# Kernel tuning notes

Measured on AMD Instinct MI355X. Metric: run time of the kernel, lower is better.

Reference implementation:

```python
import jax, jax.numpy as jnp
import numpy as np

B, T, C = 8, 2048, 1024
H, D = 16, 64  # n_heads, head_size; H*D == C


def setup_inputs() -> dict:
    key = jax.random.key(0)
    ks = jax.random.split(key, 6)
    s = 0.02
    x = jax.random.normal(ks[0], (B, T, C), dtype=jnp.float32)
    wq = jax.random.normal(ks[1], (H, C, D), dtype=jnp.float32) * s
    wk = jax.random.normal(ks[2], (H, C, D), dtype=jnp.float32) * s
    wv = jax.random.normal(ks[3], (H, C, D), dtype=jnp.float32) * s
    w_proj = jax.random.normal(ks[4], (H * D, C), dtype=jnp.float32) * s
    b_proj = jax.random.normal(ks[5], (C,), dtype=jnp.float32) * s
    return {"x": x, "wq": wq, "wk": wk, "wv": wv, "w_proj": w_proj, "b_proj": b_proj}


def reference(x, wq, wk, wv, w_proj, b_proj):
    Bq, Tq, Cq = x.shape
    # Batched per-head projections (original loops over heads with separate Linears)
    q = jnp.einsum('btc,hcd->bhtd', x, wq)
    k = jnp.einsum('btc,hcd->bhtd', x, wk)
    v = jnp.einsum('btc,hcd->bhtd', x, wv)
    # NOTE: source scales by C**-0.5 where C is the INPUT embed dim, not head_size
    wei = jnp.einsum('bhtd,bhsd->bhts', q, k) * (Cq ** -0.5)
    causal = jnp.tril(jnp.ones((Tq, Tq), dtype=bool))
    wei = jnp.where(causal, wei, jnp.float32(-jnp.inf))
    wei = jax.nn.softmax(wei, axis=-1)
    # dropout is identity in eval/reference mode
    out = jnp.einsum('bhts,bhsd->bhtd', wei, v)
    out = out.transpose(0, 2, 1, 3).reshape(Bq, Tq, H * D)  # concat over heads
    return out @ w_proj + b_proj
```

## Files before the change

kernel.cpp:

```cpp
#include <hip/hip_runtime.h>
#include <stdint.h>

#define DEV static __device__ __forceinline__

typedef __attribute__((ext_vector_type(8))) short bf16x8;
typedef __attribute__((ext_vector_type(4))) float f32x4;

constexpr int Bc = 8, Tc = 2048, Cc = 1024, Hc = 16, Dc = 64;

DEV ushort f2bf(float f) {
  union { float f; uint32_t u; } x{f};
  uint32_t r = (x.u + 0x7FFFu + ((x.u >> 16) & 1u)) >> 16;
  return (ushort)r;
}

DEV uint32_t cvt_pk_bf16(float a, float b) {
  uint32_t r;
  asm("v_cvt_pk_bf16_f32 %0, %1, %2" : "=v"(r) : "v"(a), "v"(b));
  return r;
}

DEV float max3f(float a, float b, float c) {
  float r;
  asm("v_max3_f32 %0, %1, %2, %3" : "=v"(r) : "v"(a), "v"(b), "v"(c));
  return r;
}

DEV void gload16(const ushort* g, ushort* l) {
  __builtin_amdgcn_global_load_lds(
      (const __attribute__((address_space(1))) unsigned int*)g,
      (__attribute__((address_space(3))) unsigned int*)l, 16, 0, 0);
}

DEV f32x4 mfma16(bf16x8 a, bf16x8 b, f32x4 c) {
  return __builtin_amdgcn_mfma_f32_16x16x32_bf16(a, b, c, 0, 0, 0);
}

union B8 { bf16x8 v; uint4 u; };

__global__ __launch_bounds__(256) void k_conv_x(const float* __restrict__ x, ushort* __restrict__ xb) {
  int i = blockIdx.x * 256 + threadIdx.x;
  float4 v = ((const float4*)x)[i];
  ushort4 o = make_ushort4(f2bf(v.x), f2bf(v.y), f2bf(v.z), f2bf(v.w));
  ((ushort4*)xb)[i] = o;
}

__global__ __launch_bounds__(256) void k_conv_wqkv(const float* __restrict__ wq, const float* __restrict__ wk,
                                                   const float* __restrict__ wv, ushort* __restrict__ wt) {
  int i = blockIdx.x * 256 + threadIdx.x;
  int c = i & 1023;
  int n = i >> 10;
  int which = n >> 10;
  int rem = n & 1023;
  int h = rem >> 6, d = rem & 63;
  const float* src = which == 0 ? wq : (which == 1 ? wk : wv);
  float v = src[((size_t)h * 1024 + c) * 64 + d];
  if (which == 0) v *= 0.03125f * 1.44269504088896340736f;
  wt[i] = f2bf(v);
}

__global__ __launch_bounds__(256) void k_conv_wproj(const float* __restrict__ wp, ushort* __restrict__ wt) {
  int i = blockIdx.x * 256 + threadIdx.x;
  int n = i >> 10, k = i & 1023;
  wt[i] = f2bf(wp[(size_t)k * 1024 + n]);
}

DEV void gemm_main(const ushort* __restrict__ A, const ushort* __restrict__ BT,
                   int m0, int n0, int tid, ushort* lds_a, ushort* lds_b,
                   f32x4 (&acc)[4][4]) {
  const int lane = tid & 63, wid = tid >> 6;
  const int lr = lane & 15, lg = lane >> 4;
  const int wm = wid >> 1, wn = wid & 1;
  for (int kt = 0; kt < 16; ++kt) {
#pragma unroll
    for (int r = 0; r < 4; ++r) {
      int flat = r * 256 + tid;
      int row = flat >> 3, c8 = flat & 7;
      gload16(&A[(size_t)(m0 + row) * 1024 + kt * 64 + c8 * 8], &lds_a[flat * 8]);
      gload16(&BT[(size_t)(n0 + row) * 1024 + kt * 64 + c8 * 8], &lds_b[flat * 8]);
    }
    __syncthreads();
#pragma unroll
    for (int kc = 0; kc < 2; ++kc) {
      bf16x8 af[4], bfr[4];
#pragma unroll
      for (int mf = 0; mf < 4; ++mf)
        af[mf] = *(const bf16x8*)&lds_a[(wm * 64 + mf * 16 + lr) * 64 + kc * 32 + lg * 8];
#pragma unroll
      for (int nf = 0; nf < 4; ++nf)
        bfr[nf] = *(const bf16x8*)&lds_b[(wn * 64 + nf * 16 + lr) * 64 + kc * 32 + lg * 8];
      __builtin_amdgcn_s_setprio(1);
#pragma unroll
      for (int mf = 0; mf < 4; ++mf)
#pragma unroll
        for (int nf = 0; nf < 4; ++nf)
          acc[mf][nf] = mfma16(af[mf], bfr[nf], acc[mf][nf]);
      __builtin_amdgcn_s_setprio(0);
    }
    __syncthreads();
  }
}

__global__ __launch_bounds__(256) void k_gemm_qkv(const ushort* __restrict__ xb, const ushort* __restrict__ wt,
                                                  ushort* __restrict__ qws, ushort* __restrict__ kws,
                                                  ushort* __restrict__ vws) {
  __shared__ ushort lds_a[128 * 64];
  __shared__ ushort lds_b[128 * 64];
  const int tid = threadIdx.x;
  const int m0 = blockIdx.y * 128, n0 = blockIdx.x * 128;
  f32x4 acc[4][4];
  f32x4 z = {0.f, 0.f, 0.f, 0.f};
  for (int i = 0; i < 4; ++i) for (int j = 0; j < 4; ++j) acc[i][j] = z;
  gemm_main(xb, wt, m0, n0, tid, lds_a, lds_b, acc);
  const int lane = tid & 63, wid = tid >> 6;
  const int lr = lane & 15, lg = lane >> 4;
  const int wm = wid >> 1, wn = wid & 1;
#pragma unroll
  for (int mf = 0; mf < 4; ++mf)
#pragma unroll
    for (int nf = 0; nf < 4; ++nf)
#pragma unroll
      for (int r = 0; r < 4; ++r) {
        int m = m0 + wm * 64 + mf * 16 + lg * 4 + r;
        int n = n0 + wn * 64 + nf * 16 + lr;
        int which = n >> 10, rem = n & 1023;
        int h = rem >> 6, d = rem & 63;
        int b = m >> 11, t = m & 2047;
        ushort* dst = which == 0 ? qws : (which == 1 ? kws : vws);
        dst[((size_t)(b * Hc + h) * Tc + t) * 64 + d] = f2bf(acc[mf][nf][r]);
      }
}

__global__ __launch_bounds__(256) void k_vtrans(const ushort* __restrict__ v, ushort* __restrict__ vt) {
  __shared__ ushort lds[64][68];
  const int t0 = blockIdx.x * 64;
  const int bh = blockIdx.y;
  const int tid = threadIdx.x;
  const ushort* src = v + (size_t)bh * Tc * 64;
  ushort* dst = vt + (size_t)bh * 64 * Tc;
#pragma unroll
  for (int j = 0; j < 4; ++j) {
    int flat = j * 256 + tid;
    int row = flat >> 4, cg = flat & 15;
    ushort4 x = *(const ushort4*)&src[(size_t)(t0 + row) * 64 + cg * 4];
    lds[row][cg * 4 + 0] = x.x; lds[row][cg * 4 + 1] = x.y;
    lds[row][cg * 4 + 2] = x.z; lds[row][cg * 4 + 3] = x.w;
  }
  __syncthreads();
#pragma unroll
  for (int j = 0; j < 4; ++j) {
    int flat = j * 256 + tid;
    int d = flat >> 4, tg = flat & 15;
    ushort4 x = make_ushort4(lds[tg * 4 + 0][d], lds[tg * 4 + 1][d], lds[tg * 4 + 2][d], lds[tg * 4 + 3][d]);
    *(ushort4*)&dst[(size_t)d * Tc + t0 + tg * 4] = x;
  }
}

DEV int swzK(int row, int bcol) { return row * 128 + (bcol ^ ((row & 7) << 4)); }
DEV int swzV(int row, int bcol) { return row * 256 + (bcol ^ ((row & 7) << 4)); }

__global__ __launch_bounds__(256) void k_attn(const ushort* __restrict__ qws, const ushort* __restrict__ kws,
                                              const ushort* __restrict__ vtws, ushort* __restrict__ att) {
  const int id = blockIdx.x;
  const int xcd = id & 7, slot = id >> 3;
  const int bh = (xcd << 4) + (slot >> 3);
  const int qi = slot & 7;
  const int tid = threadIdx.x, lane = tid & 63, wid = tid >> 6;
  const int lr = lane & 15, lg = lane >> 4;

  __shared__ __align__(16) ushort lds_k[2 * 128 * 64];
  __shared__ __align__(16) ushort lds_v[2 * 64 * 128];

  const ushort* qbase = qws + (size_t)bh * Tc * 64;
  const ushort* kbase = kws + (size_t)bh * Tc * 64;
  const ushort* vtbase = vtws + (size_t)bh * 64 * Tc;
  const int b = bh >> 4, h = bh & 15;
  const f32x4 z = {0.f, 0.f, 0.f, 0.f};

  int rowK[4], colK[4], rowV[4], colV[4];
#pragma unroll
  for (int r = 0; r < 4; ++r) {
    int c = r * 256 + tid;
    rowK[r] = c >> 3; colK[r] = 8 * ((c & 7) ^ (rowK[r] & 7));
    rowV[r] = c >> 4; colV[r] = 8 * ((c & 15) ^ (rowV[r] & 7));
  }

  B8 onesf;
  {
    uint32_t pp = lr == 0 ? 0x3F803F80u : 0u;
    onesf.u = make_uint4(pp, pp, pp, pp);
  }

  for (int pass = 0; pass < 2; ++pass) {
    const int qb = pass == 0 ? qi : 15 - qi;
    const int q0 = qb * 128;
    const int ntiles = qb + 1;
    const int qrow = q0 + wid * 32;
    const int qgmax = qrow + 31;

    bf16x8 qa[2][2];
#pragma unroll
    for (int qf = 0; qf < 2; ++qf)
#pragma unroll
      for (int kc = 0; kc < 2; ++kc)
        qa[qf][kc] = *(const bf16x8*)&qbase[(size_t)(qrow + qf * 16 + lr) * 64 + kc * 32 + lg * 8];

    f32x4 o[2][4];
    f32x4 lac[2];
    float m_[2];
#pragma unroll
    for (int qf = 0; qf < 2; ++qf) {
#pragma unroll
      for (int df = 0; df < 4; ++df) o[qf][df] = z;
      lac[qf] = z;
      m_[qf] = -1e30f;
    }

    __syncthreads();

#pragma unroll
    for (int r = 0; r < 4; ++r) {
      gload16(&kbase[(size_t)rowK[r] * 64 + colK[r]], &lds_k[(r * 256 + tid) * 8]);
      gload16(&vtbase[(size_t)rowV[r] * Tc + colV[r]], &lds_v[(r * 256 + tid) * 8]);
    }

    for (int it = 0; it < ntiles; ++it) {
      __syncthreads();
      const ushort* ldsK = lds_k + (it & 1) * 8192;
      const ushort* ldsV = lds_v + (it & 1) * 8192;
      if (it + 1 < ntiles) {
        const int s0n = (it + 1) * 128;
        ushort* dK = lds_k + ((it + 1) & 1) * 8192;
        ushort* dV = lds_v + ((it + 1) & 1) * 8192;
#pragma unroll
        for (int r = 0; r < 4; ++r) {
          gload16(&kbase[(size_t)(s0n + rowK[r]) * 64 + colK[r]], &dK[(r * 256 + tid) * 8]);
          gload16(&vtbase[(size_t)rowV[r] * Tc + s0n + colV[r]], &dV[(r * 256 + tid) * 8]);
        }
      }

      const int s0 = it * 128;
      const bool diag = (it == ntiles - 1);
      const int nlive = diag ? 2 * wid + 2 : 8;

      f32x4 s[8][2];
#pragma unroll
      for (int sf = 0; sf < 8; ++sf)
#pragma unroll
        for (int qf = 0; qf < 2; ++qf) s[sf][qf] = z;
#pragma unroll
      for (int kc = 0; kc < 2; ++kc) {
        bf16x8 kf[8];
#pragma unroll
        for (int sf = 0; sf < 8; ++sf)
          if (sf < nlive)
            kf[sf] = *(const bf16x8*)((const char*)ldsK + swzK(sf * 16 + lr, kc * 64 + lg * 16));
        __builtin_amdgcn_s_setprio(1);
#pragma unroll
        for (int sf = 0; sf < 8; ++sf)
          if (sf < nlive)
#pragma unroll
            for (int qf = 0; qf < 2; ++qf)
              s[sf][qf] = mfma16(kf[sf], qa[qf][kc], s[sf][qf]);
        __builtin_amdgcn_s_setprio(0);
      }

      if (diag) {
#pragma unroll
        for (int sf = 0; sf < 8; ++sf)
#pragma unroll
          for (int qf = 0; qf < 2; ++qf)
#pragma unroll
            for (int r = 0; r < 4; ++r) {
              int sg = s0 + sf * 16 + lg * 4 + r;
              int qg = qrow + qf * 16 + lr;
              if (sg > qg) s[sf][qf][r] = -1e30f;
            }
      }

      float sc[2];
      bool defer[2];
#pragma unroll
      for (int qf = 0; qf < 2; ++qf) {
        float rs[8];
#pragma unroll
        for (int sf = 0; sf < 8; ++sf)
          rs[sf] = fmaxf(max3f(s[sf][qf][0], s[sf][qf][1], s[sf][qf][2]), s[sf][qf][3]);
        float t = max3f(max3f(rs[0], rs[1], rs[2]), max3f(rs[3], rs[4], rs[5]), fmaxf(rs[6], rs[7]));
        t = fmaxf(t, __shfl_xor(t, 16));
        t = fmaxf(t, __shfl_xor(t, 32));
        defer[qf] = __all(t <= m_[qf] + 11.54f) != 0;
        float mnew = defer[qf] ? m_[qf] : fmaxf(m_[qf], t);
        sc[qf] = defer[qf] ? 1.f : exp2f(m_[qf] - mnew);
        m_[qf] = mnew;
#pragma unroll
        for (int sf = 0; sf < 8; ++sf)
#pragma unroll
          for (int r = 0; r < 4; ++r)
            s[sf][qf][r] = exp2f(s[sf][qf][r] - mnew);
      }
#pragma unroll
      for (int qf = 0; qf < 2; ++qf)
        if (!defer[qf]) {
#pragma unroll
          for (int r = 0; r < 4; ++r) {
            float scR = __shfl(sc[qf], ((lane >> 4) << 2) + r);
#pragma unroll
            for (int df = 0; df < 4; ++df) o[qf][df][r] *= scR;
            lac[qf][r] *= scR;
          }
        }

      uint32_t pk_[8][2][2];
#pragma unroll
      for (int sf = 0; sf < 8; ++sf)
#pragma unroll
        for (int qf = 0; qf < 2; ++qf) {
          pk_[sf][qf][0] = cvt_pk_bf16(s[sf][qf][0], s[sf][qf][1]);
          pk_[sf][qf][1] = cvt_pk_bf16(s[sf][qf][2], s[sf][qf][3]);
        }

#pragma unroll
      for (int kc = 0; kc < 4; ++kc) {
        B8 vf[4];
#pragma unroll
        for (int df = 0; df < 4; ++df) {
          uint2 lo = *(const uint2*)((const char*)ldsV + swzV(df * 16 + lr, kc * 64 + lg * 8));
          uint2 hi = *(const uint2*)((const char*)ldsV + swzV(df * 16 + lr, kc * 64 + 32 + lg * 8));
          vf[df].u = make_uint4(lo.x, lo.y, hi.x, hi.y);
        }
        B8 pf[2];
#pragma unroll
        for (int qf = 0; qf < 2; ++qf)
          pf[qf].u = make_uint4(pk_[2 * kc][qf][0], pk_[2 * kc][qf][1],
                                pk_[2 * kc + 1][qf][0], pk_[2 * kc + 1][qf][1]);
        __builtin_amdgcn_s_setprio(1);
#pragma unroll
        for (int qf = 0; qf < 2; ++qf) {
#pragma unroll
          for (int df = 0; df < 4; ++df)
            o[qf][df] = mfma16(pf[qf].v, vf[df].v, o[qf][df]);
          lac[qf] = mfma16(pf[qf].v, onesf.v, lac[qf]);
        }
        __builtin_amdgcn_s_setprio(0);
      }
    }

#pragma unroll
    for (int qf = 0; qf < 2; ++qf)
#pragma unroll
      for (int r = 0; r < 4; ++r) {
        float lR = __shfl(lac[qf][r], lg << 4);
        float inv = 1.f / lR;
        int qg = qrow + qf * 16 + lg * 4 + r;
#pragma unroll
        for (int df = 0; df < 4; ++df) {
          int d = df * 16 + lr;
          att[(size_t)(b * Tc + qg) * 1024 + h * 64 + d] = f2bf(o[qf][df][r] * inv);
        }
      }
  }
}

__global__ __launch_bounds__(256) void k_gemm_proj(const ushort* __restrict__ attb, const ushort* __restrict__ wt,
                                                   const float* __restrict__ bias, float* __restrict__ out) {
  __shared__ ushort lds_a[128 * 64];
  __shared__ ushort lds_b[128 * 64];
  const int tid = threadIdx.x;
  const int m0 = blockIdx.y * 128, n0 = blockIdx.x * 128;
  f32x4 acc[4][4];
  f32x4 z = {0.f, 0.f, 0.f, 0.f};
  for (int i = 0; i < 4; ++i) for (int j = 0; j < 4; ++j) acc[i][j] = z;
  gemm_main(attb, wt, m0, n0, tid, lds_a, lds_b, acc);
  const int lane = tid & 63, wid = tid >> 6;
  const int lr = lane & 15, lg = lane >> 4;
  const int wm = wid >> 1, wn = wid & 1;
#pragma unroll
  for (int mf = 0; mf < 4; ++mf)
#pragma unroll
    for (int nf = 0; nf < 4; ++nf)
#pragma unroll
      for (int r = 0; r < 4; ++r) {
        int m = m0 + wm * 64 + mf * 16 + lg * 4 + r;
        int n = n0 + wn * 64 + nf * 16 + lr;
        out[(size_t)m * 1024 + n] = acc[mf][nf][r] + bias[n];
      }
}

extern "C" void kernel_launch(void* const* d_in, const int* in_sizes, int n_in,
                              void* d_out, int out_size, void* d_ws, size_t ws_size,
                              hipStream_t stream) {
  const float* x  = (const float*)d_in[0];
  const float* wq = (const float*)d_in[1];
  const float* wk = (const float*)d_in[2];
  const float* wv = (const float*)d_in[3];
  const float* wp = (const float*)d_in[4];
  const float* bp = (const float*)d_in[5];
  float* out = (float*)d_out;

  char* ws = (char*)d_ws;
  size_t off = 0;
  auto alloc = [&](size_t bytes) { char* p = ws + off; off += (bytes + 255) & ~255ull; return p; };
  ushort* xb   = (ushort*)alloc(16384ull * 1024 * 2);
  ushort* wqkv = (ushort*)alloc(3072ull * 1024 * 2);
  ushort* wpt  = (ushort*)alloc(1024ull * 1024 * 2);
  ushort* qws  = (ushort*)alloc(16384ull * 1024 * 2);
  ushort* kws  = (ushort*)alloc(16384ull * 1024 * 2);
  ushort* vws  = (ushort*)alloc(16384ull * 1024 * 2);
  ushort* vtws = (ushort*)alloc(16384ull * 1024 * 2);
  ushort* attb = xb;

  k_conv_x<<<16384, 256, 0, stream>>>(x, xb);
  k_conv_wqkv<<<12288, 256, 0, stream>>>(wq, wk, wv, wqkv);
  k_conv_wproj<<<4096, 256, 0, stream>>>(wp, wpt);
  k_gemm_qkv<<<dim3(24, 128), 256, 0, stream>>>(xb, wqkv, qws, kws, vws);
  k_vtrans<<<dim3(32, 128), 256, 0, stream>>>(vws, vtws);
  k_attn<<<1024, 256, 0, stream>>>(qws, kws, vtws, attb);
  k_gemm_proj<<<dim3(8, 128), 256, 0, stream>>>(attb, wpt, bp, out);
}
```

Before: 544.1 us.

## Rewrite QKV and projection GEMMs with 256x256 tiles and double-buffered swizzled LDS

Replaces the 128x128 single-buffered GEMM core with a 256x256 tile per 512-thread block. The core double-buffers LDS with XOR-swizzled layout to avoid bank conflicts and interleaves prefetch of the next K-tile with MFMA work, using partial vmcnt waits and raw barriers. The block index is remapped across XCDs for L2 locality. This raises data reuse per loaded byte and hides global-load latency, but costs 128KB of LDS and many accumulator registers per block, and the fine-grained wait counts are fragile.

```diff
diff --git a/kernel.cpp b/kernel.cpp
--- a/kernel.cpp
+++ b/kernel.cpp
@@ -37,6 +37,15 @@
 }
 
 union B8 { bf16x8 v; uint4 u; };
+
+DEV void vm4() { asm volatile("s_waitcnt vmcnt(4)" ::: "memory"); }
+DEV void vm0() { asm volatile("s_waitcnt vmcnt(0)" ::: "memory"); }
+DEV void memfence() { asm volatile("" ::: "memory"); }
+DEV void pbar() {
+  __builtin_amdgcn_sched_barrier(0);
+  __builtin_amdgcn_s_barrier();
+  __builtin_amdgcn_sched_barrier(0);
+}
 
 __global__ __launch_bounds__(256) void k_conv_x(const float* __restrict__ x, ushort* __restrict__ xb) {
   int i = blockIdx.x * 256 + threadIdx.x;
@@ -65,69 +74,177 @@
   wt[i] = f2bf(wp[(size_t)k * 1024 + n]);
 }
 
-DEV void gemm_main(const ushort* __restrict__ A, const ushort* __restrict__ BT,
-                   int m0, int n0, int tid, ushort* lds_a, ushort* lds_b,
-                   f32x4 (&acc)[4][4]) {
+DEV void gemm256_main(const ushort* __restrict__ A, const ushort* __restrict__ B,
+                      int m0, int n0, int tid, ushort* ldsA, ushort* ldsB,
+                      f32x4 (&acc)[8][4]) {
+  const int lane = tid & 63;
+  const int lr = lane & 15, lg = lane >> 4;
+  const int wid = tid >> 6;
+  const int wm = wid >> 2, wn = wid & 3;
+  constexpr int NT = 16;
+
+  auto stageA = [&](int q, int t) {
+#pragma unroll
+    for (int j = 0; j < 2; ++j) {
+      int c = tid + q * 512 + j * 1024;
+      int row = c >> 3;
+      int col = 8 * ((c & 7) ^ (row & 7));
+      gload16(&A[(size_t)(m0 + row) * 1024 + t * 64 + col], &ldsA[(t & 1) * 16384 + c * 8]);
+    }
+  };
+  auto stageB = [&](int q, int t) {
+#pragma unroll
+    for (int j = 0; j < 2; ++j) {
+      int c = q * 256 + (tid & 255) + ((tid >> 8) + 2 * j) * 512;
+      int row = c >> 3;
+      int col = 8 * ((c & 7) ^ (row & 7));
+      gload16(&B[(size_t)(n0 + row) * 1024 + t * 64 + col], &ldsB[(t & 1) * 16384 + c * 8]);
+    }
+  };
+  auto rdA = [&](bf16x8 (&af)[2][4], const ushort* bA, int mh) {
+#pragma unroll
+    for (int kc = 0; kc < 2; ++kc)
+#pragma unroll
+      for (int mf = 0; mf < 4; ++mf) {
+        int row = wm * 128 + mh * 64 + mf * 16 + lr;
+        af[kc][mf] = *(const bf16x8*)((const char*)bA + row * 128 + ((kc * 64 + lg * 16) ^ ((row & 7) << 4)));
+      }
+  };
+  auto rdB = [&](bf16x8 (&bf)[2][2], const ushort* bB, int nh) {
+#pragma unroll
+    for (int kc = 0; kc < 2; ++kc)
+#pragma unroll
+      for (int nf = 0; nf < 2; ++nf) {
+        int row = wn * 64 + nh * 32 + nf * 16 + lr;
+        bf[kc][nf] = *(const bf16x8*)((const char*)bB + row * 128 + ((kc * 64 + lg * 16) ^ ((row & 7) << 4)));
+      }
+  };
+
+  stageA(0, 0); stageB(0, 0);
+  memfence();
+  stageA(1, 0); stageB(1, 0);
+  vm4();
+  pbar();
+
+  for (int t = 0; t < NT; ++t) {
+    const ushort* bA = ldsA + (t & 1) * 16384;
+    const ushort* bB = ldsB + (t & 1) * 16384;
+    const bool pf = (t + 1) < NT;
+    bf16x8 af[2][4], bf0[2][2], bf1[2][2];
+    if (pf) { stageA(0, t + 1); stageB(0, t + 1); }
+    rdA(af, bA, 0);
+    rdB(bf0, bB, 0);
+    __builtin_amdgcn_s_setprio(1);
+#pragma unroll
+    for (int kc = 0; kc < 2; ++kc)
+#pragma unroll
+      for (int mf = 0; mf < 4; ++mf)
+#pragma unroll
+        for (int nf = 0; nf < 2; ++nf)
+          acc[mf][nf] = mfma16(af[kc][mf], bf0[kc][nf], acc[mf][nf]);
+    __builtin_amdgcn_s_setprio(0);
+    if (pf) vm4(); else vm0();
+    pbar();
+    if (pf) stageA(1, t + 1);
+    rdB(bf1, bB, 1);
+    __builtin_amdgcn_s_setprio(1);
+#pragma unroll
+    for (int kc = 0; kc < 2; ++kc)
+#pragma unroll
+      for (int mf = 0; mf < 4; ++mf)
+#pragma unroll
+        for (int nf = 0; nf < 2; ++nf)
+          acc[mf][2 + nf] = mfma16(af[kc][mf], bf1[kc][nf], acc[mf][2 + nf]);
+    __builtin_amdgcn_s_setprio(0);
+    if (pf) stageB(1, t + 1);
+    rdA(af, bA, 1);
+    __builtin_amdgcn_s_setprio(1);
+#pragma unroll
+    for (int kc = 0; kc < 2; ++kc)
+#pragma unroll
+      for (int mf = 0; mf < 4; ++mf)
+#pragma unroll
+        for (int nf = 0; nf < 2; ++nf)
+          acc[4 + mf][nf] = mfma16(af[kc][mf], bf0[kc][nf], acc[4 + mf][nf]);
+    __builtin_amdgcn_s_setprio(0);
+    __builtin_amdgcn_s_setprio(1);
+#pragma unroll
+    for (int kc = 0; kc < 2; ++kc)
+#pragma unroll
+      for (int mf = 0; mf < 4; ++mf)
+#pragma unroll
+        for (int nf = 0; nf < 2; ++nf)
+          acc[4 + mf][2 + nf] = mfma16(af[kc][mf], bf1[kc][nf], acc[4 + mf][2 + nf]);
+    __builtin_amdgcn_s_setprio(0);
+    if (pf) vm4(); else vm0();
+    pbar();
+  }
+}
+
+__global__ __launch_bounds__(512, 2) void k_gemm_qkv(const ushort* __restrict__ xb, const ushort* __restrict__ wt,
+                                                     ushort* __restrict__ qws, ushort* __restrict__ kws,
+                                                     ushort* __restrict__ vws) {
+  __shared__ __align__(16) ushort ldsA[2 * 16384];
+  __shared__ __align__(16) ushort ldsB[2 * 16384];
+  const int tid = threadIdx.x;
+  const int orig = blockIdx.x;
+  const int wgid = (orig & 7) * 96 + (orig >> 3);
+  const int bn = wgid >> 6, bm = wgid & 63;
+  const int m0 = bm * 256, n0 = bn * 256;
+  f32x4 acc[8][4];
+  f32x4 z = {0.f, 0.f, 0.f, 0.f};
+#pragma unroll
+  for (int i = 0; i < 8; ++i)
+#pragma unroll
+    for (int j = 0; j < 4; ++j) acc[i][j] = z;
+  gemm256_main(xb, wt, m0, n0, tid, ldsA, ldsB, acc);
   const int lane = tid & 63, wid = tid >> 6;
   const int lr = lane & 15, lg = lane >> 4;
-  const int wm = wid >> 1, wn = wid & 1;
-  for (int kt = 0; kt < 16; ++kt) {
-#pragma unroll
-    for (int r = 0; r < 4; ++r) {
-      int flat = r * 256 + tid;
-      int row = flat >> 3, c8 = flat & 7;
-      gload16(&A[(size_t)(m0 + row) * 1024 + kt * 64 + c8 * 8], &lds_a[flat * 8]);
-      gload16(&BT[(size_t)(n0 + row) * 1024 + kt * 64 + c8 * 8], &lds_b[flat * 8]);
-    }
-    __syncthreads();
-#pragma unroll
-    for (int kc = 0; kc < 2; ++kc) {
-      bf16x8 af[4], bfr[4];
-#pragma unroll
-      for (int mf = 0; mf < 4; ++mf)
-        af[mf] = *(const bf16x8*)&lds_a[(wm * 64 + mf * 16 + lr) * 64 + kc * 32 + lg * 8];
-#pragma unroll
-      for (int nf = 0; nf < 4; ++nf)
-        bfr[nf] = *(const bf16x8*)&lds_b[(wn * 64 + nf * 16 + lr) * 64 + kc * 32 + lg * 8];
-      __builtin_amdgcn_s_setprio(1);
-#pragma unroll
-      for (int mf = 0; mf < 4; ++mf)
-#pragma unroll
-        for (int nf = 0; nf < 4; ++nf)
-          acc[mf][nf] = mfma16(af[mf], bfr[nf], acc[mf][nf]);
-      __builtin_amdgcn_s_setprio(0);
-    }
-    __syncthreads();
-  }
-}
-
-__global__ __launch_bounds__(256) void k_gemm_qkv(const ushort* __restrict__ xb, const ushort* __restrict__ wt,
-                                                  ushort* __restrict__ qws, ushort* __restrict__ kws,
-                                                  ushort* __restrict__ vws) {
-  __shared__ ushort lds_a[128 * 64];
-  __shared__ ushort lds_b[128 * 64];
-  const int tid = threadIdx.x;
-  const int m0 = blockIdx.y * 128, n0 = blockIdx.x * 128;
-  f32x4 acc[4][4];
-  f32x4 z = {0.f, 0.f, 0.f, 0.f};
-  for (int i = 0; i < 4; ++i) for (int j = 0; j < 4; ++j) acc[i][j] = z;
-  gemm_main(xb, wt, m0, n0, tid, lds_a, lds_b, acc);
-  const int lane = tid & 63, wid = tid >> 6;
-  const int lr = lane & 15, lg = lane >> 4;
-  const int wm = wid >> 1, wn = wid & 1;
-#pragma unroll
-  for (int mf = 0; mf < 4; ++mf)
+  const int wm = wid >> 2, wn = wid & 3;
+#pragma unroll
+  for (int a = 0; a < 8; ++a)
 #pragma unroll
     for (int nf = 0; nf < 4; ++nf)
 #pragma unroll
       for (int r = 0; r < 4; ++r) {
-        int m = m0 + wm * 64 + mf * 16 + lg * 4 + r;
+        int m = m0 + wm * 128 + (a >> 2) * 64 + (a & 3) * 16 + lg * 4 + r;
         int n = n0 + wn * 64 + nf * 16 + lr;
         int which = n >> 10, rem = n & 1023;
         int h = rem >> 6, d = rem & 63;
         int b = m >> 11, t = m & 2047;
         ushort* dst = which == 0 ? qws : (which == 1 ? kws : vws);
-        dst[((size_t)(b * Hc + h) * Tc + t) * 64 + d] = f2bf(acc[mf][nf][r]);
+        dst[((size_t)(b * Hc + h) * Tc + t) * 64 + d] = f2bf(acc[a][nf][r]);
+      }
+}
+
+__global__ __launch_bounds__(512, 2) void k_gemm_proj(const ushort* __restrict__ attb, const ushort* __restrict__ wt,
+                                                      const float* __restrict__ bias, float* __restrict__ out) {
+  __shared__ __align__(16) ushort ldsA[2 * 16384];
+  __shared__ __align__(16) ushort ldsB[2 * 16384];
+  const int tid = threadIdx.x;
+  const int orig = blockIdx.x;
+  const int wgid = (orig & 7) * 32 + (orig >> 3);
+  const int bn = wgid >> 6, bm = wgid & 63;
+  const int m0 = bm * 256, n0 = bn * 256;
+  f32x4 acc[8][4];
+  f32x4 z = {0.f, 0.f, 0.f, 0.f};
+#pragma unroll
+  for (int i = 0; i < 8; ++i)
+#pragma unroll
+    for (int j = 0; j < 4; ++j) acc[i][j] = z;
+  gemm256_main(attb, wt, m0, n0, tid, ldsA, ldsB, acc);
+  const int lane = tid & 63, wid = tid >> 6;
+  const int lr = lane & 15, lg = lane >> 4;
+  const int wm = wid >> 2, wn = wid & 3;
+#pragma unroll
+  for (int a = 0; a < 8; ++a)
+#pragma unroll
+    for (int nf = 0; nf < 4; ++nf)
+#pragma unroll
+      for (int r = 0; r < 4; ++r) {
+        int m = m0 + wm * 128 + (a >> 2) * 64 + (a & 3) * 16 + lg * 4 + r;
+        int n = n0 + wn * 64 + nf * 16 + lr;
+        out[(size_t)m * 1024 + n] = acc[a][nf][r] + bias[n];
       }
 }
 
@@ -360,31 +477,6 @@
         }
       }
   }
-}
-
-__global__ __launch_bounds__(256) void k_gemm_proj(const ushort* __restrict__ attb, const ushort* __restrict__ wt,
-                                                   const float* __restrict__ bias, float* __restrict__ out) {
-  __shared__ ushort lds_a[128 * 64];
-  __shared__ ushort lds_b[128 * 64];
-  const int tid = threadIdx.x;
-  const int m0 = blockIdx.y * 128, n0 = blockIdx.x * 128;
-  f32x4 acc[4][4];
-  f32x4 z = {0.f, 0.f, 0.f, 0.f};
-  for (int i = 0; i < 4; ++i) for (int j = 0; j < 4; ++j) acc[i][j] = z;
-  gemm_main(attb, wt, m0, n0, tid, lds_a, lds_b, acc);
-  const int lane = tid & 63, wid = tid >> 6;
-  const int lr = lane & 15, lg = lane >> 4;
-  const int wm = wid >> 1, wn = wid & 1;
-#pragma unroll
-  for (int mf = 0; mf < 4; ++mf)
-#pragma unroll
-    for (int nf = 0; nf < 4; ++nf)
-#pragma unroll
-      for (int r = 0; r < 4; ++r) {
-        int m = m0 + wm * 64 + mf * 16 + lg * 4 + r;
-        int n = n0 + wn * 64 + nf * 16 + lr;
-        out[(size_t)m * 1024 + n] = acc[mf][nf][r] + bias[n];
-      }
 }
 
 extern "C" void kernel_launch(void* const* d_in, const int* in_sizes, int n_in,
@@ -413,8 +505,8 @@
   k_conv_x<<<16384, 256, 0, stream>>>(x, xb);
   k_conv_wqkv<<<12288, 256, 0, stream>>>(wq, wk, wv, wqkv);
   k_conv_wproj<<<4096, 256, 0, stream>>>(wp, wpt);
-  k_gemm_qkv<<<dim3(24, 128), 256, 0, stream>>>(xb, wqkv, qws, kws, vws);
+  k_gemm_qkv<<<768, 512, 0, stream>>>(xb, wqkv, qws, kws, vws);
   k_vtrans<<<dim3(32, 128), 256, 0, stream>>>(vws, vtws);
   k_attn<<<1024, 256, 0, stream>>>(qws, kws, vtws, attb);
-  k_gemm_proj<<<dim3(8, 128), 256, 0, stream>>>(attb, wpt, bp, out);
-}
+  k_gemm_proj<<<256, 512, 0, stream>>>(attb, wpt, bp, out);
+}
```

Measured after the change: 545.1 us. No clear change (+0.2%).
